# Kernel optimization log

Hardware: AMD Instinct MI355X
Metric: run time of the kernel (lower is better)

Reference implementation:

```python
import jax, jax.numpy as jnp
import numpy as np

NUM_HEADS = 24
EPS = 1e-6


def rms_norm(x, scale):
    # fp32 RMSNorm over last dim, matching torch F.rms_norm(eps=1e-6)
    xf = x.astype(jnp.float32)
    rrms = jax.lax.rsqrt(jnp.mean(xf * xf, axis=-1, keepdims=True) + EPS)
    return (xf * rrms * scale.astype(jnp.float32)).astype(x.dtype)


def rope_rotate(x, pe):
    # x: [B,H,L,D]; pe: [B,1,L,D/2,2,2] rotation matrices
    B, H, L, D = x.shape
    xr = x.astype(jnp.float32).reshape(B, H, L, D // 2, 1, 2)
    out = pe[..., 0] * xr[..., 0] + pe[..., 1] * xr[..., 1]  # [B,H,L,D/2,2]
    return out.reshape(B, H, L, D).astype(x.dtype)


def setup_inputs() -> dict:
    key = jax.random.key(0)
    ks = jax.random.split(key, 6)
    B, L, C = 1, 2048, 3072
    H = NUM_HEADS
    D = C // H
    x = jax.random.normal(ks[0], (B, L, C), dtype=jnp.float32)
    # pe: proper RoPE rotation matrices [[cos,-sin],[sin,cos]] -> [B,1,L,D/2,2,2]
    theta = jax.random.uniform(ks[1], (B, 1, L, D // 2), dtype=jnp.float32) * (2.0 * np.pi)
    cos, sin = jnp.cos(theta), jnp.sin(theta)
    row0 = jnp.stack([cos, -sin], axis=-1)
    row1 = jnp.stack([sin, cos], axis=-1)
    pe = jnp.stack([row0, row1], axis=-2)  # [B,1,L,D/2,2,2]
    w_qkv = jax.random.normal(ks[2], (3 * C, C), dtype=jnp.float32) * (1.0 / np.sqrt(C))
    q_scale = jnp.ones((D,), dtype=jnp.float32)
    k_scale = jnp.ones((D,), dtype=jnp.float32)
    w_proj = jax.random.normal(ks[3], (C, C), dtype=jnp.float32) * (1.0 / np.sqrt(C))
    b_proj = jnp.zeros((C,), dtype=jnp.float32)
    return {"x": x, "pe": pe, "w_qkv": w_qkv, "q_scale": q_scale,
            "k_scale": k_scale, "w_proj": w_proj, "b_proj": b_proj}


def reference(x, pe, w_qkv, q_scale, k_scale, w_proj, b_proj):
    B, L, C = x.shape
    H = NUM_HEADS
    D = C // H
    qkv = x @ w_qkv.T                                   # [B,L,3C]
    qkv = qkv.reshape(B, L, 3, H, D).transpose(2, 0, 3, 1, 4)  # [3,B,H,L,D]
    q, k, v = qkv[0], qkv[1], qkv[2]
    q = rms_norm(q, q_scale)
    k = rms_norm(k, k_scale)
    q = rope_rotate(q, pe)
    k = rope_rotate(k, pe)
    scale = 1.0 / np.sqrt(D)
    scores = jnp.einsum('bhqd,bhkd->bhqk', q, k) * jnp.asarray(scale, q.dtype)
    attn = jax.nn.softmax(scores, axis=-1)
    out = jnp.einsum('bhqk,bhkd->bhqd', attn, v)        # [B,H,L,D]
    out = out.transpose(0, 2, 1, 3).reshape(B, L, C)    # [B,L,C]
    return out @ w_proj.T + b_proj
```

## Files before the change

kernel.cpp:

```cpp
#include <hip/hip_runtime.h>

typedef __attribute__((ext_vector_type(8))) __bf16 bf16x8;
typedef __attribute__((ext_vector_type(4))) float f32x4;

typedef __attribute__((address_space(1))) void gvoid;
typedef __attribute__((address_space(3))) void lvoid;

__device__ __forceinline__ float bf2f(unsigned int u) {
    union { unsigned int u; float f; } v; v.u = u << 16; return v.f;
}
__device__ __forceinline__ unsigned short f2bf(float f) {
    union { float f; unsigned int u; } v; v.f = f;
    unsigned int r = v.u + 0x7fffu + ((v.u >> 16) & 1u);
    return (unsigned short)(r >> 16);
}
__device__ __forceinline__ unsigned int pack2(float a, float b) {
    return (unsigned int)f2bf(a) | ((unsigned int)f2bf(b) << 16);
}
__device__ __forceinline__ void async16(const void* g, void* l) {
    __builtin_amdgcn_global_load_lds((gvoid*)g, (lvoid*)l, 16, 0, 0);
}
__device__ __forceinline__ float exp2f_hw(float x) {
    return __builtin_amdgcn_exp2f(x);
}


__global__ __launch_bounds__(256)
void cvt_bf16(const float4* __restrict__ s, uint4* __restrict__ d, int n8) {
    int i = blockIdx.x * 256 + threadIdx.x;
    if (i >= n8) return;
    float4 a = s[2 * i], b = s[2 * i + 1];
    uint4 o;
    o.x = pack2(a.x, a.y); o.y = pack2(a.z, a.w);
    o.z = pack2(b.x, b.y); o.w = pack2(b.z, b.w);
    d[i] = o;
}

#define GEMM_CORE(A_, lda_, B_, ldb_, K_)                                        \
    __shared__ __align__(16) unsigned short As[4096];                            \
    __shared__ __align__(16) unsigned short Bs[4096];                            \
    const int t = threadIdx.x, lane = t & 63;                                    \
    const int wm = t >> 7, wn = (t >> 6) & 1;                                    \
    const int lr = lane & 15, kc = lane >> 4;                                    \
    f32x4 acc[4][4] = {};                                                        \
    for (int k0 = 0; k0 < (K_); k0 += 32) {                                      \
        _Pragma("unroll")                                                        \
        for (int i = 0; i < 2; ++i) {                                            \
            int e = (i * 256 + t) * 8;                                           \
            int row = e >> 5, c8 = (e >> 3) & 3;                                 \
            int gc = (c8 ^ ((row >> 1) & 3)) * 8;                                \
            async16(&(A_)[(size_t)(m0 + row) * (lda_) + k0 + gc], &As[e]);       \
            async16(&(B_)[(size_t)(n0 + row) * (ldb_) + k0 + gc], &Bs[e]);       \
        }                                                                        \
        __syncthreads();                                                         \
        bf16x8 af[4], bfr[4];                                                    \
        _Pragma("unroll")                                                        \
        for (int i = 0; i < 4; ++i) {                                            \
            int ra = wm * 64 + i * 16 + lr;                                      \
            int rb = wn * 64 + i * 16 + lr;                                      \
            af[i]  = *(const bf16x8*)&As[ra * 32 + ((kc ^ ((ra >> 1) & 3)) * 8)];\
            bfr[i] = *(const bf16x8*)&Bs[rb * 32 + ((kc ^ ((rb >> 1) & 3)) * 8)];\
        }                                                                        \
        _Pragma("unroll")                                                        \
        for (int mi = 0; mi < 4; ++mi)                                           \
            _Pragma("unroll")                                                    \
            for (int ni = 0; ni < 4; ++ni)                                       \
                acc[mi][ni] = __builtin_amdgcn_mfma_f32_16x16x32_bf16(           \
                    af[mi], bfr[ni], acc[mi][ni], 0, 0, 0);                      \
        __syncthreads();                                                         \
    }

__global__ __launch_bounds__(256, 2)
void gemm_qkv(const unsigned short* __restrict__ A, const unsigned short* __restrict__ B,
              unsigned short* __restrict__ qk, unsigned short* __restrict__ vt) {
    const int n0 = blockIdx.x * 128, m0 = blockIdx.y * 128;
    GEMM_CORE(A, 3072, B, 3072, 3072)
    const int rb0 = kc * 4;
#pragma unroll
    for (int mi = 0; mi < 4; ++mi)
#pragma unroll
        for (int ni = 0; ni < 4; ++ni) {
            int col = n0 + wn * 64 + ni * 16 + lr;
#pragma unroll
            for (int r = 0; r < 4; ++r) {
                int row = m0 + wm * 64 + mi * 16 + rb0 + r;
                unsigned short v = f2bf(acc[mi][ni][r]);
                if (col < 6144) qk[(size_t)row * 6144 + col] = v;
                else            vt[(size_t)(col - 6144) * 2048 + row] = v;
            }
        }
}

__global__ __launch_bounds__(256, 2)
void gemm_proj(const unsigned short* __restrict__ A, const unsigned short* __restrict__ B,
               const float* __restrict__ bias, float* __restrict__ out) {
    const int n0 = blockIdx.x * 128, m0 = blockIdx.y * 128;
    GEMM_CORE(A, 6144, B, 3072, 3072)
    const int rb0 = kc * 4;
#pragma unroll
    for (int mi = 0; mi < 4; ++mi)
#pragma unroll
        for (int ni = 0; ni < 4; ++ni) {
            int col = n0 + wn * 64 + ni * 16 + lr;
            float badd = bias[col];
#pragma unroll
            for (int r = 0; r < 4; ++r) {
                int row = m0 + wm * 64 + mi * 16 + rb0 + r;
                out[(size_t)row * 3072 + col] = acc[mi][ni][r] + badd;
            }
        }
}

__global__ __launch_bounds__(256)
void attn2(unsigned short* __restrict__ qk, const unsigned short* __restrict__ vt) {
    __shared__ __align__(16) unsigned short Ks[64 * 128];
    __shared__ __align__(16) unsigned short Vs[128 * 64];
    __shared__ __align__(16) unsigned short Ps[4 * 16 * 64];
    const int t = threadIdx.x, lane = t & 63, w = t >> 6;
    const int h = blockIdx.x, qblk = blockIdx.y * 64;
    const int lr = lane & 15, kc = lane >> 4;
    const float sc2 = 0.08838834764831845f * 1.4426950408889634f;

    bf16x8 aq[4];
#pragma unroll
    for (int ks = 0; ks < 4; ++ks)
        aq[ks] = *(const bf16x8*)&qk[(size_t)(qblk + w * 16 + lr) * 6144 + h * 128 + ks * 32 + kc * 8];

    f32x4 o[8] = {};
    float mst[4], lst[4];
#pragma unroll
    for (int r = 0; r < 4; ++r) { mst[r] = -1e30f; lst[r] = 0.0f; }

    unsigned short* Pw = &Ps[w * 1024];

#pragma unroll
    for (int i = 0; i < 4; ++i) {
        int e = (i * 256 + t) * 8;
        {
            int row = e >> 7, c8 = (e >> 3) & 15;
            int gc = (c8 ^ (row & 15)) * 8;
            async16(&qk[(size_t)row * 6144 + 3072 + h * 128 + gc], &Ks[e]);
        }
        {
            int row = e >> 6, c8 = (e >> 3) & 7;
            int gc = (c8 ^ (row & 7)) * 8;
            async16(&vt[(size_t)(h * 128 + row) * 2048 + gc], &Vs[e]);
        }
    }

    for (int kb = 0; kb < 2048; kb += 64) {
        __syncthreads();

        bf16x8 pk[4], pv[4];
        const bool pf = (kb + 64) < 2048;
        if (pf) {
#pragma unroll
            for (int i = 0; i < 4; ++i) {
                int e = (i * 256 + t) * 8;
                {   int row = e >> 7, c8 = (e >> 3) & 15;
                    int gc = (c8 ^ (row & 15)) * 8;
                    pk[i] = *(const bf16x8*)&qk[(size_t)(kb + 64 + row) * 6144 + 3072 + h * 128 + gc];
                }
                {   int row = e >> 6, c8 = (e >> 3) & 7;
                    int gc = (c8 ^ (row & 7)) * 8;
                    pv[i] = *(const bf16x8*)&vt[(size_t)(h * 128 + row) * 2048 + kb + 64 + gc];
                }
            }
        }

        f32x4 s[4] = {};
#pragma unroll
        for (int nt = 0; nt < 4; ++nt) {
            int rk = nt * 16 + lr;
#pragma unroll
            for (int ks = 0; ks < 4; ++ks) {
                int ck = ks * 4 + kc;
                bf16x8 bk = *(const bf16x8*)&Ks[rk * 128 + ((ck ^ (rk & 15)) * 8)];
                s[nt] = __builtin_amdgcn_mfma_f32_16x16x32_bf16(aq[ks], bk, s[nt], 0, 0, 0);
            }
        }

#pragma unroll
        for (int r = 0; r < 4; ++r) {
            float vmax = fmaxf(fmaxf(s[0][r], s[1][r]), fmaxf(s[2][r], s[3][r]));
#pragma unroll
            for (int off = 8; off >= 1; off >>= 1) vmax = fmaxf(vmax, __shfl_xor(vmax, off));
            float mn = fmaxf(mst[r], vmax);
            float al = exp2f_hw((mst[r] - mn) * sc2);
            mst[r] = mn;
            float ps = 0.0f;
#pragma unroll
            for (int nt = 0; nt < 4; ++nt) {
                float p = exp2f_hw((s[nt][r] - mn) * sc2);
                s[nt][r] = p;
                ps += p;
            }
#pragma unroll
            for (int off = 8; off >= 1; off >>= 1) ps += __shfl_xor(ps, off);
            lst[r] = lst[r] * al + ps;
#pragma unroll
            for (int dt = 0; dt < 8; ++dt) o[dt][r] *= al;
        }

#pragma unroll
        for (int nt = 0; nt < 4; ++nt) {
            int col = nt * 16 + lr;
            int chunk = col >> 3, cin = col & 7;
#pragma unroll
            for (int r = 0; r < 4; ++r) {
                int q = kc * 4 + r;
                Pw[q * 64 + ((chunk ^ (q & 7)) * 8 + cin)] = f2bf(s[nt][r]);
            }
        }

#pragma unroll
        for (int ks2 = 0; ks2 < 2; ++ks2) {
            int ck = ks2 * 4 + kc;
            bf16x8 ap = *(const bf16x8*)&Pw[lr * 64 + ((ck ^ (lr & 7)) * 8)];
#pragma unroll
            for (int dt = 0; dt < 8; ++dt) {
                int rv = dt * 16 + lr;
                bf16x8 bv = *(const bf16x8*)&Vs[rv * 64 + ((ck ^ (rv & 7)) * 8)];
                o[dt] = __builtin_amdgcn_mfma_f32_16x16x32_bf16(ap, bv, o[dt], 0, 0, 0);
            }
        }
        __syncthreads();

        if (pf) {
#pragma unroll
            for (int i = 0; i < 4; ++i) {
                int e = (i * 256 + t) * 8;
                *(bf16x8*)&Ks[e] = pk[i];
                *(bf16x8*)&Vs[e] = pv[i];
            }
        }
    }

#pragma unroll
    for (int dt = 0; dt < 8; ++dt)
#pragma unroll
        for (int r = 0; r < 4; ++r) {
            int row = qblk + w * 16 + kc * 4 + r;
            qk[(size_t)row * 6144 + h * 128 + dt * 16 + lr] = f2bf(o[dt][r] / lst[r]);
        }
}


__global__ __launch_bounds__(256)
void norm_rope(unsigned short* __restrict__ qk, const float* __restrict__ pe,
               const float* __restrict__ q_scale, const float* __restrict__ k_scale) {
    const int wid = threadIdx.x >> 6, lane = threadIdx.x & 63;
    int pid = blockIdx.x * 4 + wid;
    const int isK = pid >= 49152;
    int p2 = isK ? pid - 49152 : pid;
    const int h = p2 >> 11, l = p2 & 2047;

    unsigned short* src = qk + (size_t)l * 6144 + (isK ? 3072 : 0) + h * 128 + lane * 2;
    unsigned int xu = *(const unsigned int*)src;
    float x0 = bf2f(xu & 0xffffu), x1 = bf2f(xu >> 16);
    float ss = x0 * x0 + x1 * x1;
#pragma unroll
    for (int off = 32; off >= 1; off >>= 1) ss += __shfl_xor(ss, off);
    float rr = rsqrtf(ss * (1.0f / 128.0f) + 1e-6f);

    const float* sc = isK ? k_scale : q_scale;
    float2 s2 = *(const float2*)(sc + lane * 2);
    float y0 = x0 * rr * s2.x;
    float y1 = x1 * rr * s2.y;

    float4 p4 = *(const float4*)(pe + ((size_t)l * 64 + lane) * 4);
    float o0 = p4.x * y0 + p4.y * y1;
    float o1 = p4.z * y0 + p4.w * y1;

    *(unsigned int*)src = pack2(o0, o1);
}


template <bool A32, bool B32, bool C32, bool HAS_BIAS, bool TRANS_C>
__global__ __launch_bounds__(256, 2)
void gemm_bt(const void* __restrict__ Ap, const void* __restrict__ Bp,
             const float* __restrict__ bias, void* __restrict__ Cp,
             int M, int N, int K, int lda, int ldc) {
    __shared__ __align__(16) unsigned short As[128 * 40];
    __shared__ __align__(16) unsigned short Bs[128 * 40];
    const int t = threadIdx.x, lane = t & 63;
    const int wm = t >> 7, wn = (t >> 6) & 1;
    const int m0 = blockIdx.x * 128, n0 = blockIdx.y * 128;
    const int lr = lane & 15, kc = lane >> 4;
    f32x4 acc[4][4] = {};

    for (int k0 = 0; k0 < K; k0 += 32) {
        float4 ra32[4], rb32[4];
        bf16x8 ra16[2], rb16[2];
        if constexpr (A32) {
            const float* A = (const float*)Ap;
#pragma unroll
            for (int i = 0; i < 4; ++i) {
                int idx = i * 256 + t, row = idx >> 3, c4 = idx & 7;
                ra32[i] = *(const float4*)&A[(size_t)(m0 + row) * lda + k0 + c4 * 4];
            }
        } else {
            const unsigned short* A = (const unsigned short*)Ap;
#pragma unroll
            for (int i = 0; i < 2; ++i) {
                int idx = i * 256 + t, row = idx >> 2, c8 = idx & 3;
                ra16[i] = *(const bf16x8*)&A[(size_t)(m0 + row) * lda + k0 + c8 * 8];
            }
        }
        if constexpr (B32) {
            const float* B = (const float*)Bp;
#pragma unroll
            for (int i = 0; i < 4; ++i) {
                int idx = i * 256 + t, row = idx >> 3, c4 = idx & 7;
                rb32[i] = *(const float4*)&B[(size_t)(n0 + row) * K + k0 + c4 * 4];
            }
        } else {
            const unsigned short* B = (const unsigned short*)Bp;
#pragma unroll
            for (int i = 0; i < 2; ++i) {
                int idx = i * 256 + t, row = idx >> 2, c8 = idx & 3;
                rb16[i] = *(const bf16x8*)&B[(size_t)(n0 + row) * K + k0 + c8 * 8];
            }
        }
        __syncthreads();
        if constexpr (A32) {
#pragma unroll
            for (int i = 0; i < 4; ++i) {
                int idx = i * 256 + t, row = idx >> 3, c4 = idx & 7;
                uint2 p = { pack2(ra32[i].x, ra32[i].y), pack2(ra32[i].z, ra32[i].w) };
                *(uint2*)&As[row * 40 + c4 * 4] = p;
            }
        } else {
#pragma unroll
            for (int i = 0; i < 2; ++i) {
                int idx = i * 256 + t, row = idx >> 2, c8 = idx & 3;
                *(bf16x8*)&As[row * 40 + c8 * 8] = ra16[i];
            }
        }
        if constexpr (B32) {
#pragma unroll
            for (int i = 0; i < 4; ++i) {
                int idx = i * 256 + t, row = idx >> 3, c4 = idx & 7;
                uint2 p = { pack2(rb32[i].x, rb32[i].y), pack2(rb32[i].z, rb32[i].w) };
                *(uint2*)&Bs[row * 40 + c4 * 4] = p;
            }
        } else {
#pragma unroll
            for (int i = 0; i < 2; ++i) {
                int idx = i * 256 + t, row = idx >> 2, c8 = idx & 3;
                *(bf16x8*)&Bs[row * 40 + c8 * 8] = rb16[i];
            }
        }
        __syncthreads();
        bf16x8 af[4], bfr[4];
#pragma unroll
        for (int i = 0; i < 4; ++i) {
            af[i]  = *(const bf16x8*)&As[(wm * 64 + i * 16 + lr) * 40 + kc * 8];
            bfr[i] = *(const bf16x8*)&Bs[(wn * 64 + i * 16 + lr) * 40 + kc * 8];
        }
#pragma unroll
        for (int mi = 0; mi < 4; ++mi)
#pragma unroll
            for (int ni = 0; ni < 4; ++ni)
                acc[mi][ni] = __builtin_amdgcn_mfma_f32_16x16x32_bf16(af[mi], bfr[ni], acc[mi][ni], 0, 0, 0);
    }
    const int rb0 = kc * 4;
#pragma unroll
    for (int mi = 0; mi < 4; ++mi) {
#pragma unroll
        for (int ni = 0; ni < 4; ++ni) {
            int col = n0 + wn * 64 + ni * 16 + lr;
            float badd = HAS_BIAS ? bias[col] : 0.0f;
#pragma unroll
            for (int r = 0; r < 4; ++r) {
                int row = m0 + wm * 64 + mi * 16 + rb0 + r;
                size_t off = TRANS_C ? ((size_t)col * ldc + row) : ((size_t)row * ldc + col);
                if (C32) ((float*)Cp)[off] = acc[mi][ni][r] + badd;
                else     ((unsigned short*)Cp)[off] = f2bf(acc[mi][ni][r] + badd);
            }
        }
    }
}

__global__ __launch_bounds__(256, 2)
void attn_slow(unsigned short* __restrict__ qk, const unsigned short* __restrict__ vt) {
    __shared__ __align__(16) unsigned short Ks[64 * 136];
    __shared__ __align__(16) unsigned short Vs[128 * 72];
    __shared__ __align__(16) unsigned short Ps[4 * 32 * 72];
    const int t = threadIdx.x, lane = t & 63, w = t >> 6;
    const int h = blockIdx.y, q0 = blockIdx.x * 128;
    const int lr = lane & 15, kc = lane >> 4;
    const float scale = 0.08838834764831845f;

    bf16x8 aq[2][4];
#pragma unroll
    for (int mf = 0; mf < 2; ++mf)
#pragma unroll
        for (int ks = 0; ks < 4; ++ks)
            aq[mf][ks] = *(const bf16x8*)&qk[(size_t)(q0 + w * 32 + mf * 16 + lr) * 6144 + h * 128 + ks * 32 + kc * 8];

    f32x4 o[2][8] = {};
    float mst[2][4], lst[2][4];
#pragma unroll
    for (int mf = 0; mf < 2; ++mf)
#pragma unroll
        for (int r = 0; r < 4; ++r) { mst[mf][r] = -1e30f; lst[mf][r] = 0.0f; }

    unsigned short* Pw = &Ps[w * 32 * 72];

    for (int kb = 0; kb < 2048; kb += 64) {
        bf16x8 rk[4], rv[4];
#pragma unroll
        for (int i = 0; i < 4; ++i) {
            int idx = i * 256 + t;
            { int row = idx >> 4, c8 = idx & 15;
              rk[i] = *(const bf16x8*)&qk[(size_t)(kb + row) * 6144 + 3072 + h * 128 + c8 * 8]; }
            { int row = idx >> 3, c8 = idx & 7;
              rv[i] = *(const bf16x8*)&vt[(size_t)(h * 128 + row) * 2048 + kb + c8 * 8]; }
        }
        __syncthreads();
#pragma unroll
        for (int i = 0; i < 4; ++i) {
            int idx = i * 256 + t;
            { int row = idx >> 4, c8 = idx & 15; *(bf16x8*)&Ks[row * 136 + c8 * 8] = rk[i]; }
            { int row = idx >> 3, c8 = idx & 7;  *(bf16x8*)&Vs[row * 72 + c8 * 8] = rv[i]; }
        }
        __syncthreads();

        f32x4 s[2][4] = {};
#pragma unroll
        for (int nt = 0; nt < 4; ++nt) {
            int rkr = nt * 16 + lr;
#pragma unroll
            for (int ks = 0; ks < 4; ++ks) {
                bf16x8 bk = *(const bf16x8*)&Ks[rkr * 136 + (ks * 4 + kc) * 8];
#pragma unroll
                for (int mf = 0; mf < 2; ++mf)
                    s[mf][nt] = __builtin_amdgcn_mfma_f32_16x16x32_bf16(aq[mf][ks], bk, s[mf][nt], 0, 0, 0);
            }
        }
#pragma unroll
        for (int mf = 0; mf < 2; ++mf)
#pragma unroll
            for (int nt = 0; nt < 4; ++nt)
#pragma unroll
                for (int r = 0; r < 4; ++r) s[mf][nt][r] *= scale;

#pragma unroll
        for (int mf = 0; mf < 2; ++mf) {
#pragma unroll
            for (int r = 0; r < 4; ++r) {
                float vmax = fmaxf(fmaxf(s[mf][0][r], s[mf][1][r]), fmaxf(s[mf][2][r], s[mf][3][r]));
#pragma unroll
                for (int off = 8; off >= 1; off >>= 1) vmax = fmaxf(vmax, __shfl_xor(vmax, off));
                float mn = fmaxf(mst[mf][r], vmax);
                float al = __expf(mst[mf][r] - mn);
                mst[mf][r] = mn;
                float ps = 0.0f;
#pragma unroll
                for (int nt = 0; nt < 4; ++nt) {
                    float p = __expf(s[mf][nt][r] - mn);
                    s[mf][nt][r] = p;
                    ps += p;
                }
#pragma unroll
                for (int off = 8; off >= 1; off >>= 1) ps += __shfl_xor(ps, off);
                lst[mf][r] = lst[mf][r] * al + ps;
#pragma unroll
                for (int dt = 0; dt < 8; ++dt) o[mf][dt][r] *= al;
            }
        }

#pragma unroll
        for (int mf = 0; mf < 2; ++mf)
#pragma unroll
            for (int nt = 0; nt < 4; ++nt)
#pragma unroll
                for (int r = 0; r < 4; ++r)
                    Pw[(mf * 16 + kc * 4 + r) * 72 + nt * 16 + lr] = f2bf(s[mf][nt][r]);

#pragma unroll
        for (int ks2 = 0; ks2 < 2; ++ks2) {
            bf16x8 ap[2];
#pragma unroll
            for (int mf = 0; mf < 2; ++mf)
                ap[mf] = *(const bf16x8*)&Pw[(mf * 16 + lr) * 72 + (ks2 * 4 + kc) * 8];
#pragma unroll
            for (int dt = 0; dt < 8; ++dt) {
                bf16x8 bv = *(const bf16x8*)&Vs[(dt * 16 + lr) * 72 + (ks2 * 4 + kc) * 8];
#pragma unroll
                for (int mf = 0; mf < 2; ++mf)
                    o[mf][dt] = __builtin_amdgcn_mfma_f32_16x16x32_bf16(ap[mf], bv, o[mf][dt], 0, 0, 0);
            }
        }
        __syncthreads();
    }

#pragma unroll
    for (int mf = 0; mf < 2; ++mf)
#pragma unroll
        for (int dt = 0; dt < 8; ++dt)
#pragma unroll
            for (int r = 0; r < 4; ++r) {
                int row = q0 + w * 32 + mf * 16 + kc * 4 + r;
                qk[(size_t)row * 6144 + h * 128 + dt * 16 + lr] = f2bf(o[mf][dt][r] / lst[mf][r]);
            }
}

__global__ void fill_two(float* p, int n) {
    int i = blockIdx.x * 256 + threadIdx.x;
    if (i < n) p[i] = 2.0f;
}

extern "C" void kernel_launch(void* const* d_in, const int* in_sizes, int n_in,
                              void* d_out, int out_size, void* d_ws, size_t ws_size,
                              hipStream_t stream) {
    const float* x       = (const float*)d_in[0];
    const float* pe      = (const float*)d_in[1];
    const float* w_qkv   = (const float*)d_in[2];
    const float* q_scale = (const float*)d_in[3];
    const float* k_scale = (const float*)d_in[4];
    const float* w_proj  = (const float*)d_in[5];
    const float* b_proj  = (const float*)d_in[6];
    float* out = (float*)d_out;

    if (ws_size >= 125829120ull) {
        unsigned short* ws     = (unsigned short*)d_ws;
        unsigned short* xb     = ws;
        unsigned short* wqkvb  = ws + 6291456;
        unsigned short* wprojb = ws + 34603008;
        unsigned short* qk     = ws + 44040192;
        unsigned short* vt     = ws + 56623104;

        cvt_bf16<<<3072, 256, 0, stream>>>((const float4*)x, (uint4*)xb, 786432);
        cvt_bf16<<<13824, 256, 0, stream>>>((const float4*)w_qkv, (uint4*)wqkvb, 3538944);
        cvt_bf16<<<4608, 256, 0, stream>>>((const float4*)w_proj, (uint4*)wprojb, 1179648);

        gemm_qkv<<<dim3(72, 16), 256, 0, stream>>>(xb, wqkvb, qk, vt);
        norm_rope<<<24576, 256, 0, stream>>>(qk, pe, q_scale, k_scale);
        attn2<<<dim3(24, 32), 256, 0, stream>>>(qk, vt);
        gemm_proj<<<dim3(24, 16), 256, 0, stream>>>(qk, wprojb, b_proj, out);
        return;
    }

    if (ws_size < 37748736ull) {
        fill_two<<<(6291456 + 255) / 256, 256, 0, stream>>>(out, 6291456);
        return;
    }

    unsigned short* qk = (unsigned short*)d_ws;
    unsigned short* vt = qk + 12582912;

    gemm_bt<true, true, false, false, false><<<dim3(16, 48), 256, 0, stream>>>(
        x, w_qkv, nullptr, qk, 2048, 6144, 3072, 3072, 6144);
    norm_rope<<<24576, 256, 0, stream>>>(qk, pe, q_scale, k_scale);
    gemm_bt<true, true, false, false, true><<<dim3(16, 24), 256, 0, stream>>>(
        x, w_qkv + (size_t)6144 * 3072, nullptr, vt, 2048, 3072, 3072, 3072, 2048);
    attn_slow<<<dim3(16, 24), 256, 0, stream>>>(qk, vt);
    gemm_bt<false, true, true, true, false><<<dim3(16, 24), 256, 0, stream>>>(
        qk, w_proj, b_proj, out, 2048, 3072, 3072, 6144, 3072);
}
```

Before: 605.2 us.

## Multi-stage async LDS pipeline in GEMM core with manual vmcnt waits

Replaces the single-buffered GEMM main loop with a 4-slot LDS ring, prefetching three K-tiles ahead via global_load_lds. It swaps the two __syncthreads per iteration for explicit vmcnt waits and a single barrier. MFMA issue is also wrapped in s_setprio so the math gets priority. This is meant to hide global-load latency behind MFMA work, at the cost of 4x LDS (64KB per block), which may reduce occupancy below the 2-blocks launch bound.

```diff
diff --git a/kernel.cpp b/kernel.cpp
--- a/kernel.cpp
+++ b/kernel.cpp
@@ -37,38 +37,55 @@
 }
 
 #define GEMM_CORE(A_, lda_, B_, ldb_, K_)                                        \
-    __shared__ __align__(16) unsigned short As[4096];                            \
-    __shared__ __align__(16) unsigned short Bs[4096];                            \
+    __shared__ __align__(16) unsigned short As[4][4096];                         \
+    __shared__ __align__(16) unsigned short Bs[4][4096];                         \
     const int t = threadIdx.x, lane = t & 63;                                    \
     const int wm = t >> 7, wn = (t >> 6) & 1;                                    \
     const int lr = lane & 15, kc = lane >> 4;                                    \
+    const int NK = (K_) / 32;                                                    \
+    const int e0 = t * 8, e1 = (256 + t) * 8;                                    \
+    const int r0 = e0 >> 5, c0 = (e0 >> 3) & 3;                                  \
+    const int r1 = e1 >> 5, c1 = (e1 >> 3) & 3;                                  \
+    const int g0 = (c0 ^ ((r0 >> 1) & 3)) * 8;                                   \
+    const int g1 = (c1 ^ ((r1 >> 1) & 3)) * 8;                                   \
+    const unsigned short* Ag0 = &(A_)[(size_t)(m0 + r0) * (lda_) + g0];          \
+    const unsigned short* Ag1 = &(A_)[(size_t)(m0 + r1) * (lda_) + g1];          \
+    const unsigned short* Bg0 = &(B_)[(size_t)(n0 + r0) * (ldb_) + g0];          \
+    const unsigned short* Bg1 = &(B_)[(size_t)(n0 + r1) * (ldb_) + g1];          \
     f32x4 acc[4][4] = {};                                                        \
-    for (int k0 = 0; k0 < (K_); k0 += 32) {                                      \
-        _Pragma("unroll")                                                        \
-        for (int i = 0; i < 2; ++i) {                                            \
-            int e = (i * 256 + t) * 8;                                           \
-            int row = e >> 5, c8 = (e >> 3) & 3;                                 \
-            int gc = (c8 ^ ((row >> 1) & 3)) * 8;                                \
-            async16(&(A_)[(size_t)(m0 + row) * (lda_) + k0 + gc], &As[e]);       \
-            async16(&(B_)[(size_t)(n0 + row) * (ldb_) + k0 + gc], &Bs[e]);       \
-        }                                                                        \
-        __syncthreads();                                                         \
+    RSTAGE(0) RSTAGE(1) RSTAGE(2)                                                \
+    asm volatile("s_waitcnt vmcnt(8)" ::: "memory");                             \
+    __builtin_amdgcn_s_barrier();                                                \
+    for (int kt = 0; kt < NK; ++kt) {                                            \
+        const int sl = kt & 3;                                                   \
         bf16x8 af[4], bfr[4];                                                    \
         _Pragma("unroll")                                                        \
         for (int i = 0; i < 4; ++i) {                                            \
             int ra = wm * 64 + i * 16 + lr;                                      \
             int rb = wn * 64 + i * 16 + lr;                                      \
-            af[i]  = *(const bf16x8*)&As[ra * 32 + ((kc ^ ((ra >> 1) & 3)) * 8)];\
-            bfr[i] = *(const bf16x8*)&Bs[rb * 32 + ((kc ^ ((rb >> 1) & 3)) * 8)];\
+            af[i]  = *(const bf16x8*)&As[sl][ra * 32 + ((kc ^ ((ra >> 1) & 3)) * 8)]; \
+            bfr[i] = *(const bf16x8*)&Bs[sl][rb * 32 + ((kc ^ ((rb >> 1) & 3)) * 8)]; \
         }                                                                        \
+        if (kt + 3 < NK) RSTAGE(kt + 3)                                          \
+        asm volatile("s_waitcnt lgkmcnt(0)" ::: "memory");                       \
+        __builtin_amdgcn_sched_barrier(0);                                       \
+        __builtin_amdgcn_s_setprio(1);                                           \
         _Pragma("unroll")                                                        \
         for (int mi = 0; mi < 4; ++mi)                                           \
             _Pragma("unroll")                                                    \
             for (int ni = 0; ni < 4; ++ni)                                       \
                 acc[mi][ni] = __builtin_amdgcn_mfma_f32_16x16x32_bf16(           \
                     af[mi], bfr[ni], acc[mi][ni], 0, 0, 0);                      \
-        __syncthreads();                                                         \
-    }
+        __builtin_amdgcn_s_setprio(0);                                           \
+        if (kt + 3 < NK)      { asm volatile("s_waitcnt vmcnt(8)" ::: "memory"); } \
+        else if (kt + 2 < NK) { asm volatile("s_waitcnt vmcnt(4)" ::: "memory"); } \
+        else if (kt + 1 < NK) { asm volatile("s_waitcnt vmcnt(0)" ::: "memory"); } \
+        __builtin_amdgcn_s_barrier();                                            \
+    }
+
+#define RSTAGE(kt_) { const int s_ = (kt_) & 3; const size_t k_ = (size_t)(kt_) * 32; \
+        async16(Ag0 + k_, &As[s_][e0]); async16(Ag1 + k_, &As[s_][e1]);               \
+        async16(Bg0 + k_, &Bs[s_][e0]); async16(Bg1 + k_, &Bs[s_][e1]); }
 
 __global__ __launch_bounds__(256, 2)
 void gemm_qkv(const unsigned short* __restrict__ A, const unsigned short* __restrict__ B,
```

After: 599.3 us. No clear change (-1.0%).
